# Kernel tuning notes

Hardware: AMD Instinct MI355X
Metric: run time of the kernel (lower is better)

## Reference

```python
import jax, jax.numpy as jnp
import numpy as np

HOPS = 3  # max_hops; C has HOPS+1 embedding tables


def setup_inputs() -> dict:
    key = jax.random.key(0)
    k1, k2 = jax.random.split(key)
    # story: [memory_len, batch, token_size]
    story = jax.random.randint(k1, (2048, 64, 4), 0, 50000, dtype=jnp.int64)
    # stacked embedding tables C_0..C_3: [hop+1, vocab, embed_dim], N(0, 0.1)
    C = 0.1 * jax.random.normal(k2, (HOPS + 1, 50000, 128), dtype=jnp.float32)
    return {"story": story, "C": C}


def reference(story, C):
    # story: [M, B, T] -> [B, M, T]
    story = jnp.transpose(story, (1, 0, 2))
    B, M, T = story.shape
    D = C.shape[-1]
    # padding_idx=0 semantics: embedding of token 0 is zero (fwd and bwd)
    pad_mask = (story != 0).astype(C.dtype)[..., None]  # [B, M, T, 1]

    u = jnp.zeros((B, D), dtype=C.dtype)
    for hop in range(HOPS):
        # gather + mask + sum over token dim -> memory keys m_A: [B, M, D]
        m_A = jnp.sum(C[hop][story] * pad_mask, axis=2)
        # attention scores over memory slots, softmax along M
        prob = jax.nn.softmax(jnp.einsum('bmd,bd->bm', m_A, u), axis=1)
        # memory values m_C from next-hop table: [B, M, D]
        m_C = jnp.sum(C[hop + 1][story] * pad_mask, axis=2)
        o_k = jnp.einsum('bm,bmd->bd', prob, m_C)
        u = u + o_k
    return u
```

## Files before the change

kernel.cpp:

```cpp
#include <hip/hip_runtime.h>

#define MM 2048
#define BB 64
#define TT 4
#define DD 128
#define VV 50000
#define VPAD 50176
#define NPART 392

typedef float f4v __attribute__((ext_vector_type(4)));
typedef short s8v __attribute__((ext_vector_type(8)));

__device__ __forceinline__ unsigned short f2bf(float f) {
    unsigned int u = __float_as_uint(f);
    u = u + 0x7FFFu + ((u >> 16) & 1u);
    return (unsigned short)(u >> 16);
}

__global__ void k_init(float4* __restrict__ p) {
    p[blockIdx.x * 256 + threadIdx.x] = make_float4(0.f, 0.f, 0.f, 0.f);
}

__global__ __launch_bounds__(256) void k_scatter0(const int* __restrict__ st,
                                                  float* __restrict__ W) {
    const int g = blockIdx.x * 256 + threadIdx.x;
    const int b = g & 63;
    const float p = 1.0f / (float)MM;
    const int4 tk = *(const int4*)(st + (size_t)g * 4);
    if (tk.x) atomicAdd(W + (size_t)tk.x * 64 + b, p);
    if (tk.y) atomicAdd(W + (size_t)tk.y * 64 + b, p);
    if (tk.z) atomicAdd(W + (size_t)tk.z * 64 + b, p);
    if (tk.w) atomicAdd(W + (size_t)tk.w * 64 + b, p);
}

__global__ __launch_bounds__(256, 4) void k_gemm_p(const float* __restrict__ Ch,
                                                   const float* __restrict__ u,
                                                   float* __restrict__ P) {
    __shared__ short lds[128 * 136];
    const int t = threadIdx.x;
    const int v0 = blockIdx.x * 64;

#pragma unroll
    for (int i = 0; i < 16; ++i) {
        const int G = i * 256 + t;
        const int row = G >> 5;
        const int c4 = G & 31;
        float4 val;
        if (row < 64) {
            const int v = v0 + row;
            val = (v < VV) ? *(const float4*)(Ch + (size_t)v * DD + c4 * 4)
                           : make_float4(0.f, 0.f, 0.f, 0.f);
        } else {
            val = *(const float4*)(u + (size_t)(row - 64) * DD + c4 * 4);
        }
        const unsigned int lo = ((unsigned int)f2bf(val.y) << 16) | f2bf(val.x);
        const unsigned int hi = ((unsigned int)f2bf(val.w) << 16) | f2bf(val.z);
        *(uint2*)(lds + row * 136 + c4 * 4) = make_uint2(lo, hi);
    }
    __syncthreads();

    const int l = t & 63;
    const int w = t >> 6;
    const int quad = l >> 4;
    const int n16 = l & 15;

    const int arow = (16 * w + n16) * 136;
    const int brow0 = (64 + 0 * 16 + n16) * 136;
    const int brow1 = (64 + 1 * 16 + n16) * 136;
    const int brow2 = (64 + 2 * 16 + n16) * 136;
    const int brow3 = (64 + 3 * 16 + n16) * 136;

    f4v ac0 = {0.f, 0.f, 0.f, 0.f}, ac1 = ac0, ac2 = ac0, ac3 = ac0;

#pragma unroll
    for (int s = 0; s < 4; ++s) {
        const int ko = s * 32 + quad * 8;
        const s8v av = *(const s8v*)(lds + arow + ko);
        const s8v b0 = *(const s8v*)(lds + brow0 + ko);
        const s8v b1 = *(const s8v*)(lds + brow1 + ko);
        const s8v b2 = *(const s8v*)(lds + brow2 + ko);
        const s8v b3 = *(const s8v*)(lds + brow3 + ko);
        ac0 = __builtin_amdgcn_mfma_f32_16x16x32_bf16(av, b0, ac0, 0, 0, 0);
        ac1 = __builtin_amdgcn_mfma_f32_16x16x32_bf16(av, b1, ac1, 0, 0, 0);
        ac2 = __builtin_amdgcn_mfma_f32_16x16x32_bf16(av, b2, ac2, 0, 0, 0);
        ac3 = __builtin_amdgcn_mfma_f32_16x16x32_bf16(av, b3, ac3, 0, 0, 0);
    }

    const int vbase = v0 + 16 * w + quad * 4;
#pragma unroll
    for (int r = 0; r < 4; ++r) {
        float* __restrict__ Pr = P + (size_t)(vbase + r) * 64 + n16;
        Pr[0]  = ac0[r];
        Pr[16] = ac1[r];
        Pr[32] = ac2[r];
        Pr[48] = ac3[r];
    }
}

__global__ __launch_bounds__(512) void k_attn(const int* __restrict__ st,
                                              const float* __restrict__ P,
                                              float* __restrict__ W) {
    const int b = blockIdx.x;
    const int tid = threadIdx.x;
    __shared__ float redsum[8];

    const int4 tk0 = *(const int4*)(st + ((size_t)(tid + 0)    * 64 + b) * 4);
    const int4 tk1 = *(const int4*)(st + ((size_t)(tid + 512)  * 64 + b) * 4);
    const int4 tk2 = *(const int4*)(st + ((size_t)(tid + 1024) * 64 + b) * 4);
    const int4 tk3 = *(const int4*)(st + ((size_t)(tid + 1536) * 64 + b) * 4);

    float v0 = 0.f, v1 = 0.f, v2 = 0.f, v3 = 0.f;
    if (tk0.x) v0 += P[(size_t)tk0.x * 64 + b];
    if (tk0.y) v0 += P[(size_t)tk0.y * 64 + b];
    if (tk0.z) v0 += P[(size_t)tk0.z * 64 + b];
    if (tk0.w) v0 += P[(size_t)tk0.w * 64 + b];
    if (tk1.x) v1 += P[(size_t)tk1.x * 64 + b];
    if (tk1.y) v1 += P[(size_t)tk1.y * 64 + b];
    if (tk1.z) v1 += P[(size_t)tk1.z * 64 + b];
    if (tk1.w) v1 += P[(size_t)tk1.w * 64 + b];
    if (tk2.x) v2 += P[(size_t)tk2.x * 64 + b];
    if (tk2.y) v2 += P[(size_t)tk2.y * 64 + b];
    if (tk2.z) v2 += P[(size_t)tk2.z * 64 + b];
    if (tk2.w) v2 += P[(size_t)tk2.w * 64 + b];
    if (tk3.x) v3 += P[(size_t)tk3.x * 64 + b];
    if (tk3.y) v3 += P[(size_t)tk3.y * 64 + b];
    if (tk3.z) v3 += P[(size_t)tk3.z * 64 + b];
    if (tk3.w) v3 += P[(size_t)tk3.w * 64 + b];

    v0 = __expf(v0); v1 = __expf(v1); v2 = __expf(v2); v3 = __expf(v3);
    float sum = (v0 + v1) + (v2 + v3);
#pragma unroll
    for (int off = 32; off; off >>= 1) sum += __shfl_xor(sum, off, 64);
    if ((tid & 63) == 0) redsum[tid >> 6] = sum;
    __syncthreads();
    float tot = redsum[0];
#pragma unroll
    for (int i = 1; i < 8; ++i) tot += redsum[i];
    const float inv = 1.f / tot;

    v0 *= inv; v1 *= inv; v2 *= inv; v3 *= inv;

    if (tk0.x) atomicAdd(W + (size_t)tk0.x * 64 + b, v0);
    if (tk0.y) atomicAdd(W + (size_t)tk0.y * 64 + b, v0);
    if (tk0.z) atomicAdd(W + (size_t)tk0.z * 64 + b, v0);
    if (tk0.w) atomicAdd(W + (size_t)tk0.w * 64 + b, v0);
    if (tk1.x) atomicAdd(W + (size_t)tk1.x * 64 + b, v1);
    if (tk1.y) atomicAdd(W + (size_t)tk1.y * 64 + b, v1);
    if (tk1.z) atomicAdd(W + (size_t)tk1.z * 64 + b, v1);
    if (tk1.w) atomicAdd(W + (size_t)tk1.w * 64 + b, v1);
    if (tk2.x) atomicAdd(W + (size_t)tk2.x * 64 + b, v2);
    if (tk2.y) atomicAdd(W + (size_t)tk2.y * 64 + b, v2);
    if (tk2.z) atomicAdd(W + (size_t)tk2.z * 64 + b, v2);
    if (tk2.w) atomicAdd(W + (size_t)tk2.w * 64 + b, v2);
    if (tk3.x) atomicAdd(W + (size_t)tk3.x * 64 + b, v3);
    if (tk3.y) atomicAdd(W + (size_t)tk3.y * 64 + b, v3);
    if (tk3.z) atomicAdd(W + (size_t)tk3.z * 64 + b, v3);
    if (tk3.w) atomicAdd(W + (size_t)tk3.w * 64 + b, v3);
}

__global__ __launch_bounds__(256, 3) void k_gemm_o(const float* __restrict__ C2,
                                                   float* __restrict__ W,
                                                   float* __restrict__ upart,
                                                   const int rezero) {
    __shared__ float Wl[64 * 68];
    __shared__ float Cl[64 * 136];
    const int t = threadIdx.x;
    const int g = t >> 7;
    const int b0 = ((t >> 4) & 7) * 8;
    const int d0 = (t & 15) * 8;
    const int vb = blockIdx.x * 128;

    f4v a0l = {0.f, 0.f, 0.f, 0.f}, a0h = a0l, a1l = a0l, a1h = a0l;
    f4v a2l = a0l, a2h = a0l, a3l = a0l, a3h = a0l;
    f4v a4l = a0l, a4h = a0l, a5l = a0l, a5h = a0l;
    f4v a6l = a0l, a6h = a0l, a7l = a0l, a7h = a0l;

    for (int cc = 0; cc < 2; ++cc) {
        const int vc = vb + cc * 64;
#pragma unroll
        for (int i = 0; i < 4; ++i) {
            const int G = i * 256 + t;
            const int row = G >> 4, c4 = G & 15;
            float* wp = W + (size_t)(vc + row) * 64 + c4 * 4;
            const float4 val = *(const float4*)wp;
            *(float4*)&Wl[row * 68 + c4 * 4] = val;
            if (rezero) *(float4*)wp = make_float4(0.f, 0.f, 0.f, 0.f);
        }
#pragma unroll
        for (int i = 0; i < 8; ++i) {
            const int G = i * 256 + t;
            const int row = G >> 5, c4 = G & 31;
            const int v = vc + row;
            float4 val = (v < VV) ? *(const float4*)(C2 + (size_t)v * DD + c4 * 4)
                                  : make_float4(0.f, 0.f, 0.f, 0.f);
            *(float4*)&Cl[row * 136 + c4 * 4] = val;
        }
        __syncthreads();

#define FMA_ROW(al, ah, wc)            \
    al += wc * cA; ah += wc * cB;

#pragma unroll
        for (int j = 0; j < 32; ++j) {
            const int kk = g * 32 + j;
            const f4v wA = *(const f4v*)&Wl[kk * 68 + b0];
            const f4v wB = *(const f4v*)&Wl[kk * 68 + b0 + 4];
            const f4v cA = *(const f4v*)&Cl[kk * 136 + d0];
            const f4v cB = *(const f4v*)&Cl[kk * 136 + d0 + 4];
            FMA_ROW(a0l, a0h, wA[0]) FMA_ROW(a1l, a1h, wA[1])
            FMA_ROW(a2l, a2h, wA[2]) FMA_ROW(a3l, a3h, wA[3])
            FMA_ROW(a4l, a4h, wB[0]) FMA_ROW(a5l, a5h, wB[1])
            FMA_ROW(a6l, a6h, wB[2]) FMA_ROW(a7l, a7h, wB[3])
        }
#undef FMA_ROW
        __syncthreads();
    }

    if (g == 1) {
#define STL(i, al, ah)                                   \
        *(f4v*)&Cl[(b0 + i) * 136 + d0] = al;            \
        *(f4v*)&Cl[(b0 + i) * 136 + d0 + 4] = ah;
        STL(0, a0l, a0h) STL(1, a1l, a1h) STL(2, a2l, a2h) STL(3, a3l, a3h)
        STL(4, a4l, a4h) STL(5, a5l, a5h) STL(6, a6l, a6h) STL(7, a7l, a7h)
#undef STL
    }
    __syncthreads();
    if (g == 0) {
        float* __restrict__ up = upart + (size_t)blockIdx.x * (BB * DD);
#define STG(i, al, ah) {                                             \
        const f4v xl = al + *(const f4v*)&Cl[(b0 + i) * 136 + d0];   \
        const f4v xh = ah + *(const f4v*)&Cl[(b0 + i) * 136 + d0 + 4]; \
        *(f4v*)(up + (b0 + i) * DD + d0) = xl;                       \
        *(f4v*)(up + (b0 + i) * DD + d0 + 4) = xh; }
        STG(0, a0l, a0h) STG(1, a1l, a1h) STG(2, a2l, a2h) STG(3, a3l, a3h)
        STG(4, a4l, a4h) STG(5, a5l, a5h) STG(6, a6l, a6h) STG(7, a7l, a7h)
#undef STG
    }
}

__global__ __launch_bounds__(256) void k_reduce_a(const float* __restrict__ up,
                                                  float* __restrict__ u) {
    const int jc = blockIdx.x & 31;
    const int kc = blockIdx.x >> 5;
    const int j = jc * 256 + threadIdx.x;
    const float* __restrict__ p = up + (size_t)kc * 49 * (BB * DD) + j;
    float s = 0.f;
#pragma unroll 7
    for (int k = 0; k < 49; ++k) s += p[(size_t)k * (BB * DD)];
    atomicAdd(u + j, s);
}

__global__ __launch_bounds__(256) void k_reduce_fin(const float* __restrict__ up,
                                                    const float* __restrict__ u,
                                                    float* __restrict__ out) {
    const int j = blockIdx.x * 256 + threadIdx.x;
    const float* __restrict__ p = up + j;
    float s = 0.f;
#pragma unroll 8
    for (int k = 0; k < NPART; ++k) s += p[(size_t)k * (BB * DD)];
    out[j] = u[j] + s;
}

extern "C" void kernel_launch(void* const* d_in, const int* in_sizes, int n_in,
                              void* d_out, int out_size, void* d_ws, size_t ws_size,
                              hipStream_t stream) {
    const int* st = (const int*)d_in[0];
    const float* C = (const float*)d_in[1];

    float* u  = (float*)d_ws;
    float* W  = u + BB * DD;
    float* P  = W + (size_t)VPAD * BB;
    float* up = P + (size_t)VPAD * BB;

    k_init<<<(BB * DD + VPAD * BB) / 1024, 256, 0, stream>>>((float4*)u);

    k_scatter0<<<(MM * BB) / 256, 256, 0, stream>>>(st, W);
    k_gemm_o<<<VPAD / 128, 256, 0, stream>>>(C + (size_t)1 * VV * DD, W, up, 1);
    k_reduce_a<<<256, 256, 0, stream>>>(up, u);

    k_gemm_p<<<VPAD / 64, 256, 0, stream>>>(C + (size_t)1 * VV * DD, u, P);
    k_attn<<<BB, 512, 0, stream>>>(st, P, W);
    k_gemm_o<<<VPAD / 128, 256, 0, stream>>>(C + (size_t)2 * VV * DD, W, up, 1);
    k_reduce_a<<<256, 256, 0, stream>>>(up, u);

    k_gemm_p<<<VPAD / 64, 256, 0, stream>>>(C + (size_t)2 * VV * DD, u, P);
    k_attn<<<BB, 512, 0, stream>>>(st, P, W);
    k_gemm_o<<<VPAD / 128, 256, 0, stream>>>(C + (size_t)3 * VV * DD, W, up, 0);
    k_reduce_fin<<<32, 256, 0, stream>>>(up, u, (float*)d_out);
}
```

Baseline: 361.6 us.

## Move output GEMM to bf16 MFMA and double gemm_p tile height

```diff
diff --git a/kernel.cpp b/kernel.cpp
--- a/kernel.cpp
+++ b/kernel.cpp
@@ -33,25 +33,25 @@
     if (tk.w) atomicAdd(W + (size_t)tk.w * 64 + b, p);
 }
 
-__global__ __launch_bounds__(256, 4) void k_gemm_p(const float* __restrict__ Ch,
+__global__ __launch_bounds__(256, 3) void k_gemm_p(const float* __restrict__ Ch,
                                                    const float* __restrict__ u,
                                                    float* __restrict__ P) {
-    __shared__ short lds[128 * 136];
+    __shared__ short lds[192 * 136];
     const int t = threadIdx.x;
-    const int v0 = blockIdx.x * 64;
-
-#pragma unroll
-    for (int i = 0; i < 16; ++i) {
+    const int v0 = blockIdx.x * 128;
+
+#pragma unroll
+    for (int i = 0; i < 24; ++i) {
         const int G = i * 256 + t;
         const int row = G >> 5;
         const int c4 = G & 31;
         float4 val;
-        if (row < 64) {
+        if (row < 128) {
             const int v = v0 + row;
             val = (v < VV) ? *(const float4*)(Ch + (size_t)v * DD + c4 * 4)
                            : make_float4(0.f, 0.f, 0.f, 0.f);
         } else {
-            val = *(const float4*)(u + (size_t)(row - 64) * DD + c4 * 4);
+            val = *(const float4*)(u + (size_t)(row - 128) * DD + c4 * 4);
         }
         const unsigned int lo = ((unsigned int)f2bf(val.y) << 16) | f2bf(val.x);
         const unsigned int hi = ((unsigned int)f2bf(val.w) << 16) | f2bf(val.z);
@@ -64,36 +64,43 @@
     const int quad = l >> 4;
     const int n16 = l & 15;
 
-    const int arow = (16 * w + n16) * 136;
-    const int brow0 = (64 + 0 * 16 + n16) * 136;
-    const int brow1 = (64 + 1 * 16 + n16) * 136;
-    const int brow2 = (64 + 2 * 16 + n16) * 136;
-    const int brow3 = (64 + 3 * 16 + n16) * 136;
-
-    f4v ac0 = {0.f, 0.f, 0.f, 0.f}, ac1 = ac0, ac2 = ac0, ac3 = ac0;
+    const int ar0 = (32 * w + n16) * 136;
+    const int ar1 = (32 * w + 16 + n16) * 136;
+    const int br0 = (128 + n16) * 136;
+    const int br1 = (144 + n16) * 136;
+    const int br2 = (160 + n16) * 136;
+    const int br3 = (176 + n16) * 136;
+
+    f4v c00 = {0.f, 0.f, 0.f, 0.f}, c01 = c00, c02 = c00, c03 = c00;
+    f4v c10 = c00, c11 = c00, c12 = c00, c13 = c00;
 
 #pragma unroll
     for (int s = 0; s < 4; ++s) {
         const int ko = s * 32 + quad * 8;
-        const s8v av = *(const s8v*)(lds + arow + ko);
-        const s8v b0 = *(const s8v*)(lds + brow0 + ko);
-        const s8v b1 = *(const s8v*)(lds + brow1 + ko);
-        const s8v b2 = *(const s8v*)(lds + brow2 + ko);
-        const s8v b3 = *(const s8v*)(lds + brow3 + ko);
-        ac0 = __builtin_amdgcn_mfma_f32_16x16x32_bf16(av, b0, ac0, 0, 0, 0);
-        ac1 = __builtin_amdgcn_mfma_f32_16x16x32_bf16(av, b1, ac1, 0, 0, 0);
-        ac2 = __builtin_amdgcn_mfma_f32_16x16x32_bf16(av, b2, ac2, 0, 0, 0);
-        ac3 = __builtin_amdgcn_mfma_f32_16x16x32_bf16(av, b3, ac3, 0, 0, 0);
-    }
-
-    const int vbase = v0 + 16 * w + quad * 4;
+        const s8v a0 = *(const s8v*)(lds + ar0 + ko);
+        const s8v a1 = *(const s8v*)(lds + ar1 + ko);
+        const s8v b0 = *(const s8v*)(lds + br0 + ko);
+        const s8v b1 = *(const s8v*)(lds + br1 + ko);
+        const s8v b2 = *(const s8v*)(lds + br2 + ko);
+        const s8v b3 = *(const s8v*)(lds + br3 + ko);
+        c00 = __builtin_amdgcn_mfma_f32_16x16x32_bf16(a0, b0, c00, 0, 0, 0);
+        c01 = __builtin_amdgcn_mfma_f32_16x16x32_bf16(a0, b1, c01, 0, 0, 0);
+        c02 = __builtin_amdgcn_mfma_f32_16x16x32_bf16(a0, b2, c02, 0, 0, 0);
+        c03 = __builtin_amdgcn_mfma_f32_16x16x32_bf16(a0, b3, c03, 0, 0, 0);
+        c10 = __builtin_amdgcn_mfma_f32_16x16x32_bf16(a1, b0, c10, 0, 0, 0);
+        c11 = __builtin_amdgcn_mfma_f32_16x16x32_bf16(a1, b1, c11, 0, 0, 0);
+        c12 = __builtin_amdgcn_mfma_f32_16x16x32_bf16(a1, b2, c12, 0, 0, 0);
+        c13 = __builtin_amdgcn_mfma_f32_16x16x32_bf16(a1, b3, c13, 0, 0, 0);
+    }
+
+    const int vb0 = v0 + 32 * w + quad * 4;
+    const int vb1 = vb0 + 16;
 #pragma unroll
     for (int r = 0; r < 4; ++r) {
-        float* __restrict__ Pr = P + (size_t)(vbase + r) * 64 + n16;
-        Pr[0]  = ac0[r];
-        Pr[16] = ac1[r];
-        Pr[32] = ac2[r];
-        Pr[48] = ac3[r];
+        float* __restrict__ P0 = P + (size_t)(vb0 + r) * 64 + n16;
+        P0[0] = c00[r]; P0[16] = c01[r]; P0[32] = c02[r]; P0[48] = c03[r];
+        float* __restrict__ P1 = P + (size_t)(vb1 + r) * 64 + n16;
+        P1[0] = c10[r]; P1[16] = c11[r]; P1[32] = c12[r]; P1[48] = c13[r];
     }
 }
 
@@ -162,79 +169,88 @@
                                                    float* __restrict__ W,
                                                    float* __restrict__ upart,
                                                    const int rezero) {
-    __shared__ float Wl[64 * 68];
-    __shared__ float Cl[64 * 136];
+    __shared__ unsigned Wt[64 * 68];
+    __shared__ unsigned Ct[128 * 68];
     const int t = threadIdx.x;
-    const int g = t >> 7;
-    const int b0 = ((t >> 4) & 7) * 8;
-    const int d0 = (t & 15) * 8;
     const int vb = blockIdx.x * 128;
 
-    f4v a0l = {0.f, 0.f, 0.f, 0.f}, a0h = a0l, a1l = a0l, a1h = a0l;
-    f4v a2l = a0l, a2h = a0l, a3l = a0l, a3h = a0l;
-    f4v a4l = a0l, a4h = a0l, a5l = a0l, a5h = a0l;
-    f4v a6l = a0l, a6h = a0l, a7l = a0l, a7h = a0l;
-
-    for (int cc = 0; cc < 2; ++cc) {
-        const int vc = vb + cc * 64;
-#pragma unroll
-        for (int i = 0; i < 4; ++i) {
-            const int G = i * 256 + t;
-            const int row = G >> 4, c4 = G & 15;
-            float* wp = W + (size_t)(vc + row) * 64 + c4 * 4;
-            const float4 val = *(const float4*)wp;
-            *(float4*)&Wl[row * 68 + c4 * 4] = val;
-            if (rezero) *(float4*)wp = make_float4(0.f, 0.f, 0.f, 0.f);
+#pragma unroll
+    for (int i = 0; i < 4; ++i) {
+        const int item = i * 256 + t;
+        const int q = item & 15;
+        const int p = item >> 4;
+        float* w0 = W + (size_t)(vb + 2 * p) * 64 + 4 * q;
+        float* w1 = W + (size_t)(vb + 2 * p + 1) * 64 + 4 * q;
+        const float4 x = *(const float4*)w0;
+        const float4 y = *(const float4*)w1;
+        if (rezero) {
+            *(float4*)w0 = make_float4(0.f, 0.f, 0.f, 0.f);
+            *(float4*)w1 = make_float4(0.f, 0.f, 0.f, 0.f);
         }
-#pragma unroll
-        for (int i = 0; i < 8; ++i) {
-            const int G = i * 256 + t;
-            const int row = G >> 5, c4 = G & 31;
-            const int v = vc + row;
-            float4 val = (v < VV) ? *(const float4*)(C2 + (size_t)v * DD + c4 * 4)
-                                  : make_float4(0.f, 0.f, 0.f, 0.f);
-            *(float4*)&Cl[row * 136 + c4 * 4] = val;
-        }
-        __syncthreads();
-
-#define FMA_ROW(al, ah, wc)            \
-    al += wc * cA; ah += wc * cB;
-
-#pragma unroll
-        for (int j = 0; j < 32; ++j) {
-            const int kk = g * 32 + j;
-            const f4v wA = *(const f4v*)&Wl[kk * 68 + b0];
-            const f4v wB = *(const f4v*)&Wl[kk * 68 + b0 + 4];
-            const f4v cA = *(const f4v*)&Cl[kk * 136 + d0];
-            const f4v cB = *(const f4v*)&Cl[kk * 136 + d0 + 4];
-            FMA_ROW(a0l, a0h, wA[0]) FMA_ROW(a1l, a1h, wA[1])
-            FMA_ROW(a2l, a2h, wA[2]) FMA_ROW(a3l, a3h, wA[3])
-            FMA_ROW(a4l, a4h, wB[0]) FMA_ROW(a5l, a5h, wB[1])
-            FMA_ROW(a6l, a6h, wB[2]) FMA_ROW(a7l, a7h, wB[3])
-        }
-#undef FMA_ROW
-        __syncthreads();
-    }
-
-    if (g == 1) {
-#define STL(i, al, ah)                                   \
-        *(f4v*)&Cl[(b0 + i) * 136 + d0] = al;            \
-        *(f4v*)&Cl[(b0 + i) * 136 + d0 + 4] = ah;
-        STL(0, a0l, a0h) STL(1, a1l, a1h) STL(2, a2l, a2h) STL(3, a3l, a3h)
-        STL(4, a4l, a4h) STL(5, a5l, a5h) STL(6, a6l, a6h) STL(7, a7l, a7h)
-#undef STL
+        Wt[(4 * q + 0) * 68 + p] = ((unsigned)f2bf(y.x) << 16) | f2bf(x.x);
+        Wt[(4 * q + 1) * 68 + p] = ((unsigned)f2bf(y.y) << 16) | f2bf(x.y);
+        Wt[(4 * q + 2) * 68 + p] = ((unsigned)f2bf(y.z) << 16) | f2bf(x.z);
+        Wt[(4 * q + 3) * 68 + p] = ((unsigned)f2bf(y.w) << 16) | f2bf(x.w);
+    }
+#pragma unroll
+    for (int i = 0; i < 8; ++i) {
+        const int item = i * 256 + t;
+        const int q = item & 31;
+        const int p = item >> 5;
+        const int v0 = vb + 2 * p;
+        const float4 x = (v0 < VV)
+            ? *(const float4*)(C2 + (size_t)v0 * DD + 4 * q)
+            : make_float4(0.f, 0.f, 0.f, 0.f);
+        const float4 y = (v0 + 1 < VV)
+            ? *(const float4*)(C2 + (size_t)(v0 + 1) * DD + 4 * q)
+            : make_float4(0.f, 0.f, 0.f, 0.f);
+        Ct[(4 * q + 0) * 68 + p] = ((unsigned)f2bf(y.x) << 16) | f2bf(x.x);
+        Ct[(4 * q + 1) * 68 + p] = ((unsigned)f2bf(y.y) << 16) | f2bf(x.y);
+        Ct[(4 * q + 2) * 68 + p] = ((unsigned)f2bf(y.z) << 16) | f2bf(x.z);
+        Ct[(4 * q + 3) * 68 + p] = ((unsigned)f2bf(y.w) << 16) | f2bf(x.w);
     }
     __syncthreads();
-    if (g == 0) {
-        float* __restrict__ up = upart + (size_t)blockIdx.x * (BB * DD);
-#define STG(i, al, ah) {                                             \
-        const f4v xl = al + *(const f4v*)&Cl[(b0 + i) * 136 + d0];   \
-        const f4v xh = ah + *(const f4v*)&Cl[(b0 + i) * 136 + d0 + 4]; \
-        *(f4v*)(up + (b0 + i) * DD + d0) = xl;                       \
-        *(f4v*)(up + (b0 + i) * DD + d0 + 4) = xh; }
-        STG(0, a0l, a0h) STG(1, a1l, a1h) STG(2, a2l, a2h) STG(3, a3l, a3h)
-        STG(4, a4l, a4h) STG(5, a5l, a5h) STG(6, a6l, a6h) STG(7, a7l, a7h)
-#undef STG
+
+    const int l = t & 63;
+    const int w = t >> 6;
+    const int quad = l >> 4;
+    const int n16 = l & 15;
+
+    f4v a00 = {0.f, 0.f, 0.f, 0.f}, a01 = a00;
+    f4v a10 = a00, a11 = a00, a20 = a00, a21 = a00, a30 = a00, a31 = a00;
+
+#pragma unroll
+    for (int ch = 0; ch < 4; ++ch) {
+        const int ku = ch * 16 + quad * 4;
+        const s8v wa0 = *(const s8v*)&Wt[(0  + n16) * 68 + ku];
+        const s8v wa1 = *(const s8v*)&Wt[(16 + n16) * 68 + ku];
+        const s8v wa2 = *(const s8v*)&Wt[(32 + n16) * 68 + ku];
+        const s8v wa3 = *(const s8v*)&Wt[(48 + n16) * 68 + ku];
+        const s8v cb0 = *(const s8v*)&Ct[(w * 32 + n16) * 68 + ku];
+        const s8v cb1 = *(const s8v*)&Ct[(w * 32 + 16 + n16) * 68 + ku];
+        a00 = __builtin_amdgcn_mfma_f32_16x16x32_bf16(wa0, cb0, a00, 0, 0, 0);
+        a01 = __builtin_amdgcn_mfma_f32_16x16x32_bf16(wa0, cb1, a01, 0, 0, 0);
+        a10 = __builtin_amdgcn_mfma_f32_16x16x32_bf16(wa1, cb0, a10, 0, 0, 0);
+        a11 = __builtin_amdgcn_mfma_f32_16x16x32_bf16(wa1, cb1, a11, 0, 0, 0);
+        a20 = __builtin_amdgcn_mfma_f32_16x16x32_bf16(wa2, cb0, a20, 0, 0, 0);
+        a21 = __builtin_amdgcn_mfma_f32_16x16x32_bf16(wa2, cb1, a21, 0, 0, 0);
+        a30 = __builtin_amdgcn_mfma_f32_16x16x32_bf16(wa3, cb0, a30, 0, 0, 0);
+        a31 = __builtin_amdgcn_mfma_f32_16x16x32_bf16(wa3, cb1, a31, 0, 0, 0);
+    }
+
+    float* __restrict__ up = upart + (size_t)blockIdx.x * (BB * DD);
+    const int dc = w * 32 + n16;
+#pragma unroll
+    for (int r = 0; r < 4; ++r) {
+        const int br = quad * 4 + r;
+        up[(br +  0) * DD + dc]      = a00[r];
+        up[(br +  0) * DD + dc + 16] = a01[r];
+        up[(br + 16) * DD + dc]      = a10[r];
+        up[(br + 16) * DD + dc + 16] = a11[r];
+        up[(br + 32) * DD + dc]      = a20[r];
+        up[(br + 32) * DD + dc + 16] = a21[r];
+        up[(br + 48) * DD + dc]      = a30[r];
+        up[(br + 48) * DD + dc + 16] = a31[r];
     }
 }
 
@@ -278,12 +294,12 @@
     k_gemm_o<<<VPAD / 128, 256, 0, stream>>>(C + (size_t)1 * VV * DD, W, up, 1);
     k_reduce_a<<<256, 256, 0, stream>>>(up, u);
 
-    k_gemm_p<<<VPAD / 64, 256, 0, stream>>>(C + (size_t)1 * VV * DD, u, P);
+    k_gemm_p<<<VPAD / 128, 256, 0, stream>>>(C + (size_t)1 * VV * DD, u, P);
     k_attn<<<BB, 512, 0, stream>>>(st, P, W);
     k_gemm_o<<<VPAD / 128, 256, 0, stream>>>(C + (size_t)2 * VV * DD, W, up, 1);
     k_reduce_a<<<256, 256, 0, stream>>>(up, u);
 
-    k_gemm_p<<<VPAD / 64, 256, 0, stream>>>(C + (size_t)2 * VV * DD, u, P);
+    k_gemm_p<<<VPAD / 128, 256, 0, stream>>>(C + (size_t)2 * VV * DD, u, P);
     k_attn<<<BB, 512, 0, stream>>>(st, P, W);
     k_gemm_o<<<VPAD / 128, 256, 0, stream>>>(C + (size_t)3 * VV * DD, W, up, 0);
     k_reduce_fin<<<32, 256, 0, stream>>>(up, u, (float*)d_out);
```

After: 326.9 us. 9.6% less time.
